# Kernel tuning notes

Measured on AMD Instinct MI355X. Metric: run time of the kernel, lower is better.

## Reference

```python
import jax, jax.numpy as jnp
import numpy as np

N, E, G = 30000, 240000, 128
D_IN, D_H, D_OUT, HEADS = 128, 128, 16, 4
EPS_BN = 1e-5


def setup_inputs() -> dict:
    key = jax.random.key(0)
    ks = jax.random.split(key, 24)
    s = 0.1
    inp = {
        "x": jax.random.normal(ks[0], (N, D_IN), jnp.float32),
        "edge_index": jax.random.randint(ks[1], (2, E), 0, N, jnp.int32),
        "batch": jnp.sort(jax.random.randint(ks[2], (N,), 0, G, jnp.int32)),
        # stacked per-layer params (3 GAT blocks, identical shapes since D_IN==D_H)
        "W": jax.random.normal(ks[3], (3, D_H, HEADS * D_H), jnp.float32) * s,
        "att_src": jax.random.normal(ks[4], (3, HEADS, D_H), jnp.float32) * s,
        "att_dst": jax.random.normal(ks[5], (3, HEADS, D_H), jnp.float32) * s,
        "conv_b": jnp.zeros((3, D_H), jnp.float32),
        "gamma": jnp.ones((3, D_H), jnp.float32),
        "beta": jnp.zeros((3, D_H), jnp.float32),
        "sk_Win": jax.random.normal(ks[6], (3, D_H, D_H), jnp.float32) * s,
        "sk_bin": jnp.zeros((3, D_H), jnp.float32),
        "sk_Wout": jax.random.normal(ks[7], (3, D_H, D_H), jnp.float32) * s,
        "sk_bout": jnp.zeros((3, D_H), jnp.float32),
        "fc1_W": jax.random.normal(ks[8], (D_H, D_H), jnp.float32) * s,
        "fc1_b": jnp.zeros((D_H,), jnp.float32),
        "fc3_W": jax.random.normal(ks[9], (D_H, D_OUT), jnp.float32) * s,
        "fc3_b": jnp.zeros((D_OUT,), jnp.float32),
    }
    return inp


def _gat_conv(x, src, dst, W, a_src, a_dst, b):
    # PyG GATConv, heads=4, concat=False (mean over heads), leaky_relu 0.2
    h = (x @ W).reshape(N, HEADS, D_H)                      # [N,H,C]
    al_s = jnp.einsum('nhc,hc->nh', h, a_src)               # [N,H]
    al_d = jnp.einsum('nhc,hc->nh', h, a_dst)
    e = jax.nn.leaky_relu(al_s[src] + al_d[dst], 0.2)       # [Etot,H]
    m = jax.ops.segment_max(e, dst, num_segments=N)
    m = jnp.where(jnp.isfinite(m), m, 0.0)
    ex = jnp.exp(e - m[dst])
    z = jax.ops.segment_sum(ex, dst, num_segments=N)
    alpha = ex / (z[dst] + 1e-16)                           # [Etot,H]
    msg = h[src] * alpha[:, :, None]                        # [Etot,H,C]
    out = jax.ops.segment_sum(msg, dst, num_segments=N)     # [N,H,C]
    return out.mean(axis=1) + b


def _batch_norm(h, gamma, beta):
    mu = h.mean(axis=0)
    var = h.var(axis=0)
    return gamma * (h - mu) * jax.lax.rsqrt(var + EPS_BN) + beta


def _gated_skip(in_x, out_x, Win, bin_, Wout, bout):
    gate = jax.nn.sigmoid(in_x @ Win + bin_ + out_x @ Wout + bout)
    return gate * out_x + (1.0 - gate) * in_x


def reference(x, edge_index, batch, W, att_src, att_dst, conv_b, gamma, beta,
              sk_Win, sk_bin, sk_Wout, sk_bout, fc1_W, fc1_b, fc3_W, fc3_b):
    # add self loops (PyG GATConv default)
    loops = jnp.arange(N, dtype=edge_index.dtype)
    src = jnp.concatenate([edge_index[0], loops])
    dst = jnp.concatenate([edge_index[1], loops])

    h = x
    for l in range(3):
        idn = h
        h = _gat_conv(h, src, dst, W[l], att_src[l], att_dst[l], conv_b[l])
        h = _batch_norm(h, gamma[l], beta[l])
        h = _gated_skip(idn, h, sk_Win[l], sk_bin[l], sk_Wout[l], sk_bout[l])
        h = jax.nn.relu(h)

    # global mean pool over graphs
    cnt = jax.ops.segment_sum(jnp.ones((N,), h.dtype), batch, num_segments=G)
    hg = jax.ops.segment_sum(h, batch, num_segments=G) / jnp.maximum(cnt, 1.0)[:, None]
    hg = jax.nn.relu(hg @ fc1_W + fc1_b)
    return hg @ fc3_W + fc3_b
```

## Files before the change

### kernel.cpp

```cpp
#include <hip/hip_runtime.h>
#include <hip/hip_bf16.h>

#define N_NODES 30000
#define N_EDGES 240000
#define ETOT    (N_EDGES + N_NODES)
#define NGRAPH  128
#define NBLK    118

typedef __attribute__((ext_vector_type(8))) short bf16x8;
typedef __attribute__((ext_vector_type(4))) short bf16x4;
typedef __attribute__((ext_vector_type(4))) float f32x4;

__device__ __forceinline__ unsigned short f2bf(float f) {
    unsigned u = __float_as_uint(f);
    u += 0x7fff + ((u >> 16) & 1);
    return (unsigned short)(u >> 16);
}
__device__ __forceinline__ float bf2f(unsigned short h) {
    return __uint_as_float(((unsigned)h) << 16);
}

__global__ __launch_bounds__(256) void prep_kernel(const float* __restrict__ W,
                                                   const float* __restrict__ Win,
                                                   const float* __restrict__ Wout,
                                                   const float* __restrict__ x,
                                                   const int* __restrict__ batch,
                                                   short* __restrict__ wt_hi,
                                                   short* __restrict__ wint_hi,
                                                   short* __restrict__ woutt_hi,
                                                   short* __restrict__ xb,
                                                   int* __restrict__ gstart) {
    int i = blockIdx.x * 256 + threadIdx.x;
    if (i < 196608) {
        int l = i >> 16, r = i & 65535;
        int n = r >> 7, k = r & 127;
        wt_hi[i] = (short)f2bf(W[(size_t)l * 65536 + k * 512 + n]);
    } else if (i < 245760) {
        int j = i - 196608;
        int l = j >> 14, r = j & 16383;
        int n = r >> 7, k = r & 127;
        wint_hi[j] = (short)f2bf(Win[(size_t)l * 16384 + k * 128 + n]);
    } else if (i < 294912) {
        int j = i - 245760;
        int l = j >> 14, r = j & 16383;
        int n = r >> 7, k = r & 127;
        woutt_hi[j] = (short)f2bf(Wout[(size_t)l * 16384 + k * 128 + n]);
    } else if (i < 294912 + 480000) {
        int j = i - 294912;
        const float4* p = (const float4*)x + (size_t)j * 2;
        float4 v0 = p[0], v1 = p[1];
        bf16x8 hv;
        hv[0] = (short)f2bf(v0.x); hv[1] = (short)f2bf(v0.y);
        hv[2] = (short)f2bf(v0.z); hv[3] = (short)f2bf(v0.w);
        hv[4] = (short)f2bf(v1.x); hv[5] = (short)f2bf(v1.y);
        hv[6] = (short)f2bf(v1.z); hv[7] = (short)f2bf(v1.w);
        *(bf16x8*)(xb + (size_t)j * 8) = hv;
    } else if (i < 294912 + 480000 + 129) {
        int t = i - 294912 - 480000;
        int lo = 0, hi = N_NODES;
        while (lo < hi) { int mid = (lo + hi) >> 1; if (batch[mid] < t) lo = mid + 1; else hi = mid; }
        gstart[t] = lo;
    }
}

__global__ __launch_bounds__(256) void gemm_conv(const short* __restrict__ Ab,
                                                 const short* __restrict__ Bth,
                                                 const float* __restrict__ att_s,
                                                 const float* __restrict__ att_d,
                                                 unsigned short* __restrict__ hfullb,
                                                 float* __restrict__ als,
                                                 float* __restrict__ ald) {
    __shared__ short As_h[64 * 136];
    __shared__ float red_s[2][64], red_d[2][64];
    const int bm = blockIdx.x * 64;
    const int hd = blockIdx.y;
    const int bn = hd * 128;
    const int t  = threadIdx.x;
#pragma unroll
    for (int i = 0; i < 4; i++) {
        int idx8 = t + i * 256;
        int row = idx8 >> 4, c8 = (idx8 & 15) << 3;
        bf16x8 vh = {};
        if (bm + row < N_NODES)
            vh = *(const bf16x8*)(Ab + (size_t)(bm + row) * 128 + c8);
        *(bf16x8*)(As_h + row * 136 + c8) = vh;
    }
    __syncthreads();

    const int w = t >> 6, lane = t & 63;
    const int wr = w >> 1, wc = w & 1;
    const int lr = lane & 15, lg = lane >> 4;
    f32x4 acc[2][4] = {};
    const size_t bofs0 = (size_t)(bn + wc * 64 + lr) * 128 + lg * 8;
#pragma unroll
    for (int kk = 0; kk < 4; kk++) {
        bf16x8 ah[2], bh[4];
#pragma unroll
        for (int ni = 0; ni < 4; ni++) {
            size_t o = bofs0 + (size_t)ni * 16 * 128 + kk * 32;
            bh[ni] = *(const bf16x8*)(Bth + o);
        }
        int ko = kk * 32 + lg * 8;
#pragma unroll
        for (int mi = 0; mi < 2; mi++) {
            int r = wr * 32 + mi * 16 + lr;
            ah[mi] = *(const bf16x8*)(As_h + r * 136 + ko);
        }
#pragma unroll
        for (int mi = 0; mi < 2; mi++)
#pragma unroll
            for (int ni = 0; ni < 4; ni++)
                acc[mi][ni] = __builtin_amdgcn_mfma_f32_16x16x32_bf16(ah[mi], bh[ni], acc[mi][ni], 0, 0, 0);
    }
    float as_c[4], ad_c[4];
#pragma unroll
    for (int ni = 0; ni < 4; ni++) {
        int cc = wc * 64 + ni * 16 + lr;
        as_c[ni] = att_s[hd * 128 + cc];
        ad_c[ni] = att_d[hd * 128 + cc];
    }
#pragma unroll
    for (int mi = 0; mi < 2; mi++) {
#pragma unroll
        for (int r = 0; r < 4; r++) {
            float ps = 0.f, pd = 0.f;
#pragma unroll
            for (int ni = 0; ni < 4; ni++) {
                ps = fmaf(acc[mi][ni][r], as_c[ni], ps);
                pd = fmaf(acc[mi][ni][r], ad_c[ni], pd);
            }
#pragma unroll
            for (int off = 1; off < 16; off <<= 1) {
                ps += __shfl_xor(ps, off);
                pd += __shfl_xor(pd, off);
            }
            if (lr == 0) {
                int row = wr * 32 + mi * 16 + lg * 4 + r;
                red_s[wc][row] = ps;
                red_d[wc][row] = pd;
            }
        }
    }
    __syncthreads();
#pragma unroll
    for (int mi = 0; mi < 2; mi++)
#pragma unroll
        for (int ni = 0; ni < 4; ni++) {
            int nl = wc * 64 + ni * 16 + lr;
#pragma unroll
            for (int r = 0; r < 4; r++) {
                int row = wr * 32 + mi * 16 + lg * 4 + r;
                As_h[row * 136 + nl] = (short)f2bf(acc[mi][ni][r]);
            }
        }
    if (t < 64) {
        int m = bm + t;
        if (m < N_NODES) als[m * 4 + hd] = red_s[0][t] + red_s[1][t];
    } else if (t < 128) {
        int tt = t - 64;
        int m = bm + tt;
        if (m < N_NODES) ald[m * 4 + hd] = red_d[0][tt] + red_d[1][tt];
    }
    __syncthreads();
#pragma unroll
    for (int i2 = 0; i2 < 4; i2++) {
        int idx8 = t + i2 * 256;
        int row = idx8 >> 4, c8 = (idx8 & 15) << 3;
        int m = bm + row;
        if (m < N_NODES)
            *(bf16x8*)(hfullb + (size_t)m * 512 + bn + c8) = *(const bf16x8*)(As_h + row * 136 + c8);
    }
}

__global__ __launch_bounds__(256) void skip_conv(const short* __restrict__ hinb,
                                                 const float* __restrict__ g,
                                                 const float* __restrict__ bnsum,
                                                 const float* __restrict__ gamma,
                                                 const float* __restrict__ beta,
                                                 const short* __restrict__ w1h,
                                                 const short* __restrict__ w2h,
                                                 const float* __restrict__ bin,
                                                 const float* __restrict__ bout,
                                                 const short* __restrict__ wtn,
                                                 const float* __restrict__ att_s,
                                                 const float* __restrict__ att_d,
                                                 short* __restrict__ houtb,
                                                 unsigned short* __restrict__ hfullb,
                                                 float* __restrict__ als,
                                                 float* __restrict__ ald) {
    __shared__ short A1h[64 * 136], A2h[64 * 136];
    __shared__ float bnp_s[256];
    __shared__ float redS[4][64], redD[4][64];
    const int bm = blockIdx.x * 64;
    const int t  = threadIdx.x;
    if (t < 128) {
        float inv = 1.f / (float)N_NODES;
        float mu  = bnsum[t] * inv;
        float var = bnsum[128 + t] * inv - mu * mu;
        float rs  = rsqrtf(var + 1e-5f);
        float sc  = gamma[t] * rs;
        bnp_s[t]       = sc;
        bnp_s[128 + t] = beta[t] - mu * sc;
    }
    __syncthreads();
#pragma unroll
    for (int i = 0; i < 4; i++) {
        int idx8 = t + i * 256;
        int row = idx8 >> 4, c8 = (idx8 & 15) << 3;
        bf16x8 vh = {};
        if (bm + row < N_NODES)
            vh = *(const bf16x8*)(hinb + (size_t)(bm + row) * 128 + c8);
        *(bf16x8*)(A1h + row * 136 + c8) = vh;
    }
#pragma unroll
    for (int i = 0; i < 8; i++) {
        int idx4 = t + i * 256;
        int row = idx4 >> 5, c4 = (idx4 & 31) << 2;
        float4 v2 = make_float4(0.f, 0.f, 0.f, 0.f);
        if (bm + row < N_NODES) {
            float4 gv = *(const float4*)(g + (size_t)(bm + row) * 128 + c4);
            v2.x = fmaf(bnp_s[c4 + 0], gv.x, bnp_s[128 + c4 + 0]);
            v2.y = fmaf(bnp_s[c4 + 1], gv.y, bnp_s[128 + c4 + 1]);
            v2.z = fmaf(bnp_s[c4 + 2], gv.z, bnp_s[128 + c4 + 2]);
            v2.w = fmaf(bnp_s[c4 + 3], gv.w, bnp_s[128 + c4 + 3]);
        }
        *(bf16x4*)(A2h + row * 136 + c4) = (bf16x4){(short)f2bf(v2.x), (short)f2bf(v2.y),
                                                    (short)f2bf(v2.z), (short)f2bf(v2.w)};
    }
    __syncthreads();

    const int w = t >> 6, lane = t & 63;
    const int wr = w >> 1, wc = w & 1;
    const int lr = lane & 15, lg = lane >> 4;

    {
        f32x4 acc[2][4] = {};
        const size_t bo = (size_t)(wc * 64 + lr) * 128 + lg * 8;
#pragma unroll
        for (int kk = 0; kk < 4; kk++) {
            bf16x8 a1[2], a2[2], b1[4], b2[4];
#pragma unroll
            for (int ni = 0; ni < 4; ni++) {
                size_t o = bo + (size_t)ni * 2048 + kk * 32;
                b1[ni] = *(const bf16x8*)(w1h + o);
                b2[ni] = *(const bf16x8*)(w2h + o);
            }
            int ko = kk * 32 + lg * 8;
#pragma unroll
            for (int mi = 0; mi < 2; mi++) {
                int r = wr * 32 + mi * 16 + lr;
                a1[mi] = *(const bf16x8*)(A1h + r * 136 + ko);
                a2[mi] = *(const bf16x8*)(A2h + r * 136 + ko);
            }
#pragma unroll
            for (int mi = 0; mi < 2; mi++)
#pragma unroll
                for (int ni = 0; ni < 4; ni++) {
                    acc[mi][ni] = __builtin_amdgcn_mfma_f32_16x16x32_bf16(a1[mi], b1[ni], acc[mi][ni], 0, 0, 0);
                    acc[mi][ni] = __builtin_amdgcn_mfma_f32_16x16x32_bf16(a2[mi], b2[ni], acc[mi][ni], 0, 0, 0);
                }
        }
#pragma unroll
        for (int mi = 0; mi < 2; mi++)
#pragma unroll
            for (int ni = 0; ni < 4; ni++) {
                int n = wc * 64 + ni * 16 + lr;
                float bsum = bin[n] + bout[n];
                float sc = bnp_s[n], shb = bnp_s[128 + n];
#pragma unroll
                for (int r = 0; r < 4; r++) {
                    int lrow = wr * 32 + mi * 16 + lg * 4 + r;
                    int m = bm + lrow;
                    float gv = (m < N_NODES) ? g[(size_t)m * 128 + n] : 0.f;
                    float hbnv = fmaf(sc, gv, shb);
                    float hv   = bf2f((unsigned short)A1h[lrow * 136 + n]);
                    float gt   = 1.f / (1.f + __expf(-(acc[mi][ni][r] + bsum)));
                    acc[mi][ni][r] = fmaxf(gt * hbnv + (1.f - gt) * hv, 0.f);
                }
            }
        __syncthreads();
#pragma unroll
        for (int mi = 0; mi < 2; mi++)
#pragma unroll
            for (int ni = 0; ni < 4; ni++) {
                int n = wc * 64 + ni * 16 + lr;
#pragma unroll
                for (int r = 0; r < 4; r++) {
                    int lrow = wr * 32 + mi * 16 + lg * 4 + r;
                    A1h[lrow * 136 + n] = (short)f2bf(acc[mi][ni][r]);
                }
            }
        __syncthreads();
#pragma unroll
        for (int i2 = 0; i2 < 4; i2++) {
            int idx8 = t + i2 * 256;
            int row = idx8 >> 4, c8 = (idx8 & 15) << 3;
            int m = bm + row;
            if (m < N_NODES)
                *(bf16x8*)(houtb + (size_t)m * 128 + c8) = *(const bf16x8*)(A1h + row * 136 + c8);
        }
    }

    f32x4 c2[4][8] = {};
    const int hd = w;
    const size_t bo2 = (size_t)(hd * 128 + lr) * 128 + lg * 8;
#pragma unroll
    for (int kk = 0; kk < 4; kk++) {
        bf16x8 ah2[4], bh2[8];
#pragma unroll
        for (int ni = 0; ni < 8; ni++)
            bh2[ni] = *(const bf16x8*)(wtn + bo2 + (size_t)ni * 2048 + kk * 32);
        int ko = kk * 32 + lg * 8;
#pragma unroll
        for (int mi = 0; mi < 4; mi++)
            ah2[mi] = *(const bf16x8*)(A1h + (mi * 16 + lr) * 136 + ko);
#pragma unroll
        for (int mi = 0; mi < 4; mi++)
#pragma unroll
            for (int ni = 0; ni < 8; ni++)
                c2[mi][ni] = __builtin_amdgcn_mfma_f32_16x16x32_bf16(ah2[mi], bh2[ni], c2[mi][ni], 0, 0, 0);
    }
    {
        float asc[8], adc[8];
#pragma unroll
        for (int ni = 0; ni < 8; ni++) {
            int cc = ni * 16 + lr;
            asc[ni] = att_s[hd * 128 + cc];
            adc[ni] = att_d[hd * 128 + cc];
        }
#pragma unroll
        for (int mi = 0; mi < 4; mi++)
#pragma unroll
            for (int r = 0; r < 4; r++) {
                float ps = 0.f, pd = 0.f;
#pragma unroll
                for (int ni = 0; ni < 8; ni++) {
                    ps = fmaf(c2[mi][ni][r], asc[ni], ps);
                    pd = fmaf(c2[mi][ni][r], adc[ni], pd);
                }
#pragma unroll
                for (int off = 1; off < 16; off <<= 1) {
                    ps += __shfl_xor(ps, off);
                    pd += __shfl_xor(pd, off);
                }
                if (lr == 0) {
                    int row = mi * 16 + lg * 4 + r;
                    redS[hd][row] = ps;
                    redD[hd][row] = pd;
                }
            }
    }
    __syncthreads();
    if (w < 2) {
        short* dst = (w == 0) ? A1h : A2h;
#pragma unroll
        for (int mi = 0; mi < 4; mi++)
#pragma unroll
            for (int ni = 0; ni < 8; ni++)
#pragma unroll
                for (int r = 0; r < 4; r++)
                    dst[(mi * 16 + lg * 4 + r) * 136 + ni * 16 + lr] = (short)f2bf(c2[mi][ni][r]);
    }
    {
        int hd2 = t >> 6, row = t & 63;
        int m = bm + row;
        if (m < N_NODES) {
            als[m * 4 + hd2] = redS[hd2][row];
            ald[m * 4 + hd2] = redD[hd2][row];
        }
    }
    __syncthreads();
#pragma unroll
    for (int it = 0; it < 8; it++) {
        int idx = t + it * 256;
        int row = idx >> 5, c8 = (idx & 31) << 3;
        int m = bm + row;
        if (m < N_NODES) {
            const short* src = (c8 < 128) ? A1h : A2h;
            *(bf16x8*)(hfullb + (size_t)m * 512 + c8) = *(const bf16x8*)(src + row * 136 + (c8 & 127));
        }
    }
    __syncthreads();
    if (w >= 2) {
        short* dst = (w == 2) ? A1h : A2h;
#pragma unroll
        for (int mi = 0; mi < 4; mi++)
#pragma unroll
            for (int ni = 0; ni < 8; ni++)
#pragma unroll
                for (int r = 0; r < 4; r++)
                    dst[(mi * 16 + lg * 4 + r) * 136 + ni * 16 + lr] = (short)f2bf(c2[mi][ni][r]);
    }
    __syncthreads();
#pragma unroll
    for (int it = 0; it < 8; it++) {
        int idx = t + it * 256;
        int row = idx >> 5, c8 = (idx & 31) << 3;
        int m = bm + row;
        if (m < N_NODES) {
            const short* src = (c8 < 128) ? A1h : A2h;
            *(bf16x8*)(hfullb + (size_t)m * 512 + 256 + c8) = *(const bf16x8*)(src + row * 136 + (c8 & 127));
        }
    }
}

__global__ __launch_bounds__(256) void skip_gate(const short* __restrict__ hinb,
                                                 const float* __restrict__ g,
                                                 const float* __restrict__ bnsum,
                                                 const float* __restrict__ gamma,
                                                 const float* __restrict__ beta,
                                                 const short* __restrict__ w1h,
                                                 const short* __restrict__ w2h,
                                                 const float* __restrict__ bin, const float* __restrict__ bout,
                                                 short* __restrict__ houtb) {
    __shared__ short A1h[64 * 136], A2h[64 * 136], A2l[64 * 136];
    __shared__ float bnp_s[256];
    const int bm = blockIdx.x * 64;
    const int bn = blockIdx.y * 64;
    const int t  = threadIdx.x;
    if (t < 128) {
        float inv = 1.f / (float)N_NODES;
        float mu  = bnsum[t] * inv;
        float var = bnsum[128 + t] * inv - mu * mu;
        float rs  = rsqrtf(var + 1e-5f);
        float sc  = gamma[t] * rs;
        bnp_s[t]       = sc;
        bnp_s[128 + t] = beta[t] - mu * sc;
    }
    __syncthreads();
#pragma unroll
    for (int i = 0; i < 4; i++) {
        int idx8 = t + i * 256;
        int row = idx8 >> 4, c8 = (idx8 & 15) << 3;
        bf16x8 vh = {};
        if (bm + row < N_NODES)
            vh = *(const bf16x8*)(hinb + (size_t)(bm + row) * 128 + c8);
        *(bf16x8*)(A1h + row * 136 + c8) = vh;
    }
#pragma unroll
    for (int i = 0; i < 8; i++) {
        int idx4 = t + i * 256;
        int row = idx4 >> 5, c4 = (idx4 & 31) << 2;
        float4 v2 = make_float4(0.f, 0.f, 0.f, 0.f);
        if (bm + row < N_NODES) {
            float4 gv = *(const float4*)(g + (size_t)(bm + row) * 128 + c4);
            v2.x = fmaf(bnp_s[c4 + 0], gv.x, bnp_s[128 + c4 + 0]);
            v2.y = fmaf(bnp_s[c4 + 1], gv.y, bnp_s[128 + c4 + 1]);
            v2.z = fmaf(bnp_s[c4 + 2], gv.z, bnp_s[128 + c4 + 2]);
            v2.w = fmaf(bnp_s[c4 + 3], gv.w, bnp_s[128 + c4 + 3]);
        }
        unsigned short b0 = f2bf(v2.x), b1 = f2bf(v2.y), b2 = f2bf(v2.z), b3 = f2bf(v2.w);
        *(bf16x4*)(A2h + row * 136 + c4) = (bf16x4){(short)b0, (short)b1, (short)b2, (short)b3};
        *(bf16x4*)(A2l + row * 136 + c4) = (bf16x4){(short)f2bf(v2.x - bf2f(b0)), (short)f2bf(v2.y - bf2f(b1)),
                                                    (short)f2bf(v2.z - bf2f(b2)), (short)f2bf(v2.w - bf2f(b3))};
    }
    __syncthreads();

    const int w = t >> 6, lane = t & 63;
    const int wr = w >> 1, wc = w & 1;
    const int lr = lane & 15, lg = lane >> 4;
    f32x4 acc[2][2] = {};
    const size_t bofs0 = (size_t)(bn + wc * 32 + lr) * 128 + lg * 8;
#pragma unroll
    for (int kk = 0; kk < 4; kk++) {
        bf16x8 a1f[2], a2f[2], b1h[2], b2h[2];
#pragma unroll
        for (int ni = 0; ni < 2; ni++) {
            size_t o = bofs0 + (size_t)ni * 16 * 128 + kk * 32;
            b1h[ni] = *(const bf16x8*)(w1h + o);
            b2h[ni] = *(const bf16x8*)(w2h + o);
        }
        int ko = kk * 32 + lg * 8;
#pragma unroll
        for (int mi = 0; mi < 2; mi++) {
            int r = wr * 32 + mi * 16 + lr;
            a1f[mi] = *(const bf16x8*)(A1h + r * 136 + ko);
            a2f[mi] = *(const bf16x8*)(A2h + r * 136 + ko);
        }
#pragma unroll
        for (int mi = 0; mi < 2; mi++)
#pragma unroll
            for (int ni = 0; ni < 2; ni++) {
                acc[mi][ni] = __builtin_amdgcn_mfma_f32_16x16x32_bf16(a1f[mi], b1h[ni], acc[mi][ni], 0, 0, 0);
                acc[mi][ni] = __builtin_amdgcn_mfma_f32_16x16x32_bf16(a2f[mi], b2h[ni], acc[mi][ni], 0, 0, 0);
            }
    }
#pragma unroll
    for (int mi = 0; mi < 2; mi++) {
#pragma unroll
        for (int ni = 0; ni < 2; ni++) {
            int n = bn + wc * 32 + ni * 16 + lr;
            float bsum = bin[n] + bout[n];
#pragma unroll
            for (int r = 0; r < 4; r++) {
                int lrow = wr * 32 + mi * 16 + lg * 4 + r;
                float hbnv = bf2f((unsigned short)A2h[lrow * 136 + n]) + bf2f((unsigned short)A2l[lrow * 136 + n]);
                float hv   = bf2f((unsigned short)A1h[lrow * 136 + n]);
                float gt   = 1.f / (1.f + __expf(-(acc[mi][ni][r] + bsum)));
                acc[mi][ni][r] = fmaxf(gt * hbnv + (1.f - gt) * hv, 0.f);
            }
        }
    }
    __syncthreads();
#pragma unroll
    for (int mi = 0; mi < 2; mi++)
#pragma unroll
        for (int ni = 0; ni < 2; ni++) {
            int n = bn + wc * 32 + ni * 16 + lr;
#pragma unroll
            for (int r = 0; r < 4; r++) {
                int lrow = wr * 32 + mi * 16 + lg * 4 + r;
                A1h[lrow * 136 + n] = (short)f2bf(acc[mi][ni][r]);
            }
        }
    __syncthreads();
#pragma unroll
    for (int i2 = 0; i2 < 2; i2++) {
        int idx8 = t + i2 * 256;
        int row = idx8 >> 3, c8 = (idx8 & 7) << 3;
        int m = bm + row;
        if (m < N_NODES)
            *(bf16x8*)(houtb + (size_t)m * 128 + bn + c8) = *(const bf16x8*)(A1h + row * 136 + bn + c8);
    }
}

__global__ __launch_bounds__(256) void deg_kernel(const int* __restrict__ ei1,
                                                  int* __restrict__ deg) {
    int e = blockIdx.x * 256 + threadIdx.x;
    if (e >= ETOT) return;
    int d = (e < N_EDGES) ? ei1[e] : (e - N_EDGES);
    atomicAdd(&deg[d], 1);
}

__global__ __launch_bounds__(256) void scan1(const int* __restrict__ deg,
                                             int* __restrict__ tmp,
                                             int* __restrict__ blksum) {
    int i = blockIdx.x * 256 + threadIdx.x;
    int v = (i < N_NODES) ? deg[i] : 0;
    __shared__ int sh[256];
    sh[threadIdx.x] = v;
    __syncthreads();
    int acc = v;
    for (int off = 1; off < 256; off <<= 1) {
        int u = (threadIdx.x >= off) ? sh[threadIdx.x - off] : 0;
        __syncthreads();
        acc += u;
        sh[threadIdx.x] = acc;
        __syncthreads();
    }
    if (i < N_NODES) tmp[i] = acc - v;
    if (threadIdx.x == 255) blksum[blockIdx.x] = acc;
}

__global__ void scan2(const int* __restrict__ blksum, int* __restrict__ blkoff) {
    int t = threadIdx.x;
    int v = (t < NBLK) ? blksum[t] : 0;
    __shared__ int sh[128];
    sh[t] = v;
    __syncthreads();
    int acc = v;
    for (int off = 1; off < 128; off <<= 1) {
        int u = (t >= off) ? sh[t - off] : 0;
        __syncthreads();
        acc += u;
        sh[t] = acc;
        __syncthreads();
    }
    if (t < NBLK) blkoff[t] = acc - v;
}

__global__ __launch_bounds__(256) void scan3(const int* __restrict__ tmp,
                                             const int* __restrict__ blkoff,
                                             int* __restrict__ rowptr,
                                             int* __restrict__ wofs) {
    int i = blockIdx.x * 256 + threadIdx.x;
    if (i == 0) rowptr[N_NODES] = ETOT;
    if (i < N_NODES) {
        int r = tmp[i] + blkoff[blockIdx.x];
        rowptr[i] = r;
        wofs[i]   = r;
    }
}

__global__ __launch_bounds__(256) void scatter_kernel(const int* __restrict__ ei0,
                                                      const int* __restrict__ ei1,
                                                      int* __restrict__ wofs,
                                                      int* __restrict__ csr_src) {
    int e = blockIdx.x * 256 + threadIdx.x;
    if (e >= ETOT) return;
    int s = (e < N_EDGES) ? ei0[e] : (e - N_EDGES);
    int d = (e < N_EDGES) ? ei1[e] : (e - N_EDGES);
    int pos = atomicAdd(&wofs[d], 1);
    csr_src[pos] = s;
}

__global__ __launch_bounds__(256) void gat_gather(const int* __restrict__ rowptr,
                                                  const int* __restrict__ csr_src,
                                                  const float* __restrict__ al_s,
                                                  const float* __restrict__ al_d,
                                                  const unsigned short* __restrict__ hfullb,
                                                  const float* __restrict__ conv_b,
                                                  float* __restrict__ g,
                                                  float* __restrict__ bnsum,
                                                  float* __restrict__ bnsum2) {
    const int lane = threadIdx.x & 63;
    const int wib  = threadIdx.x >> 6;
    const int gwid = blockIdx.x * 4 + wib;
    const int nw   = gridDim.x * 4;
    const int h    = lane >> 4;
    const int sub  = lane & 15;
    float s1[8] = {}, s2[8] = {};

    for (int n = gwid; n < N_NODES; n += nw) {
        const int e0 = rowptr[n], e1 = rowptr[n + 1];
        const float ald_h = al_d[n * 4 + h];

        float acc[8] = {};
        float zs = 0.f;
        int i = e0;
        for (; i + 3 < e1; i += 4) {
            int sA = csr_src[i], sB = csr_src[i + 1], sC = csr_src[i + 2], sD = csr_src[i + 3];
            bf16x8 ha = *(const bf16x8*)(hfullb + (size_t)sA * 512 + lane * 8);
            bf16x8 hb = *(const bf16x8*)(hfullb + (size_t)sB * 512 + lane * 8);
            bf16x8 hc = *(const bf16x8*)(hfullb + (size_t)sC * 512 + lane * 8);
            bf16x8 hd = *(const bf16x8*)(hfullb + (size_t)sD * 512 + lane * 8);
            float vA = al_s[sA * 4 + h] + ald_h; vA = (vA > 0.f) ? vA : 0.2f * vA;
            float vB = al_s[sB * 4 + h] + ald_h; vB = (vB > 0.f) ? vB : 0.2f * vB;
            float vC = al_s[sC * 4 + h] + ald_h; vC = (vC > 0.f) ? vC : 0.2f * vC;
            float vD = al_s[sD * 4 + h] + ald_h; vD = (vD > 0.f) ? vD : 0.2f * vD;
            float exA = __expf(vA), exB = __expf(vB), exC = __expf(vC), exD = __expf(vD);
            zs += (exA + exB) + (exC + exD);
#pragma unroll
            for (int j = 0; j < 8; j++) {
                float a = fmaf(exA, bf2f((unsigned short)ha[j]), acc[j]);
                a = fmaf(exB, bf2f((unsigned short)hb[j]), a);
                a = fmaf(exC, bf2f((unsigned short)hc[j]), a);
                acc[j] = fmaf(exD, bf2f((unsigned short)hd[j]), a);
            }
        }
        for (; i < e1; i++) {
            int sA = csr_src[i];
            bf16x8 ha = *(const bf16x8*)(hfullb + (size_t)sA * 512 + lane * 8);
            float vA = al_s[sA * 4 + h] + ald_h; vA = (vA > 0.f) ? vA : 0.2f * vA;
            float exA = __expf(vA);
            zs += exA;
#pragma unroll
            for (int j = 0; j < 8; j++)
                acc[j] = fmaf(exA, bf2f((unsigned short)ha[j]), acc[j]);
        }

        float inv = 0.25f / (zs + 1e-16f);
#pragma unroll
        for (int j = 0; j < 8; j++) {
            float a = acc[j] * inv;
            a += __shfl_xor(a, 16);
            a += __shfl_xor(a, 32);
            acc[j] = a;
        }
        if (lane < 16) {
            float o[8];
#pragma unroll
            for (int j = 0; j < 8; j++) {
                float tv = acc[j] + conv_b[sub * 8 + j];
                o[j] = tv;
                s1[j] += tv;
                s2[j] = fmaf(tv, tv, s2[j]);
            }
            float* gp = g + (size_t)n * 128 + sub * 8;
            *(float4*)gp       = make_float4(o[0], o[1], o[2], o[3]);
            *(float4*)(gp + 4) = make_float4(o[4], o[5], o[6], o[7]);
        }
    }

    __shared__ float redA[4][128], redB[4][128];
    if (lane < 16) {
#pragma unroll
        for (int j = 0; j < 8; j++) {
            redA[wib][sub * 8 + j] = s1[j];
            redB[wib][sub * 8 + j] = s2[j];
        }
    }
    __syncthreads();
    int t = threadIdx.x;
    if (t < 128) {
        atomicAdd(&bnsum[t], redA[0][t] + redA[1][t] + redA[2][t] + redA[3][t]);
    } else {
        int c = t - 128;
        atomicAdd(&bnsum2[c], redB[0][c] + redB[1][c] + redB[2][c] + redB[3][c]);
    }
}

__global__ __launch_bounds__(256) void pool_head(const short* __restrict__ hb,
                                                 const int* __restrict__ gstart,
                                                 const float* __restrict__ fc1W,
                                                 const float* __restrict__ fc1b,
                                                 const float* __restrict__ fc3W,
                                                 const float* __restrict__ fc3b,
                                                 float* __restrict__ out) {
    int gid = blockIdx.x, t = threadIdx.x;
    int lo = gstart[gid], hi = gstart[gid + 1];
    int c = t & 127, half = t >> 7;
    float s = 0.f;
    for (int n = lo + half; n < hi; n += 2)
        s += bf2f((unsigned short)hb[(size_t)n * 128 + c]);
    __shared__ float sh[256];
    __shared__ float hg[128], a1[128];
    sh[t] = s;
    __syncthreads();
    if (half == 0) {
        float cc = fmaxf((float)(hi - lo), 1.f);
        hg[c] = (sh[c] + sh[c + 128]) / cc;
    }
    __syncthreads();
    if (t < 128) {
        float v = fc1b[t];
        for (int c2 = 0; c2 < 128; c2++) v = fmaf(hg[c2], fc1W[c2 * 128 + t], v);
        a1[t] = fmaxf(v, 0.f);
    }
    __syncthreads();
    if (t < 16) {
        float o = fc3b[t];
        for (int j = 0; j < 128; j++) o = fmaf(a1[j], fc3W[j * 16 + t], o);
        out[gid * 16 + t] = o;
    }
}

extern "C" void kernel_launch(void* const* d_in, const int* in_sizes, int n_in,
                              void* d_out, int out_size, void* d_ws, size_t ws_size,
                              hipStream_t stream) {
    const float* x       = (const float*)d_in[0];
    const int*   ei      = (const int*)d_in[1];
    const int*   batch   = (const int*)d_in[2];
    const float* W       = (const float*)d_in[3];
    const float* att_src = (const float*)d_in[4];
    const float* att_dst = (const float*)d_in[5];
    const float* conv_b  = (const float*)d_in[6];
    const float* gamma   = (const float*)d_in[7];
    const float* beta    = (const float*)d_in[8];
    const float* sk_Win  = (const float*)d_in[9];
    const float* sk_bin  = (const float*)d_in[10];
    const float* sk_Wout = (const float*)d_in[11];
    const float* sk_bout = (const float*)d_in[12];
    const float* fc1_W   = (const float*)d_in[13];
    const float* fc1_b   = (const float*)d_in[14];
    const float* fc3_W   = (const float*)d_in[15];
    const float* fc3_b   = (const float*)d_in[16];
    float* out = (float*)d_out;
    const int* ei0 = ei;
    const int* ei1 = ei + N_EDGES;

    float* ws = (float*)d_ws;
    size_t o = 0;
    unsigned short* hfullb = (unsigned short*)(ws + o); o += (size_t)N_NODES * 256;
    float* gbuf   = ws + o; o += (size_t)N_NODES * 128;
    short* hbA    = (short*)(ws + o); o += (size_t)N_NODES * 64;
    short* hbB    = (short*)(ws + o); o += (size_t)N_NODES * 64;
    float* als    = ws + o; o += N_NODES * 4;
    float* ald    = ws + o; o += N_NODES * 4;
    float* bnsum  = ws + o; o += 768;
    short* wt_hi   = (short*)(ws + o); o += 98304;
    short* wint_hi = (short*)(ws + o); o += 24576;
    short* woutt_hi = (short*)(ws + o); o += 24576;
    int* gstart   = (int*)(ws + o); o += 132;
    int* deg      = (int*)(ws + o); o += N_NODES;
    int* rowptr   = (int*)(ws + o); o += N_NODES + 4;
    int* wofs     = (int*)(ws + o); o += N_NODES;
    int* scantmp  = (int*)(ws + o); o += N_NODES;
    int* blksum   = (int*)(ws + o); o += NBLK + 2;
    int* blkoff   = (int*)(ws + o); o += NBLK + 2;
    int* csr_src  = (int*)(ws + o); o += ETOT;

    prep_kernel<<<3028, 256, 0, stream>>>(W, sk_Win, sk_Wout, x, batch,
                                          wt_hi, wint_hi, woutt_hi, hbA, gstart);

    hipMemsetAsync(deg, 0, N_NODES * 4, stream);
    hipMemsetAsync(bnsum, 0, 768 * 4, stream);
    deg_kernel<<<(ETOT + 255) / 256, 256, 0, stream>>>(ei1, deg);
    scan1<<<NBLK, 256, 0, stream>>>(deg, scantmp, blksum);
    scan2<<<1, 128, 0, stream>>>(blksum, blkoff);
    scan3<<<NBLK, 256, 0, stream>>>(scantmp, blkoff, rowptr, wofs);
    scatter_kernel<<<(ETOT + 255) / 256, 256, 0, stream>>>(ei0, ei1, wofs, csr_src);

    gemm_conv<<<dim3(469, 4), 256, 0, stream>>>(hbA, wt_hi, att_src, att_dst, hfullb, als, ald);
    gat_gather<<<1024, 256, 0, stream>>>(rowptr, csr_src, als, ald, hfullb,
                                         conv_b, gbuf, bnsum, bnsum + 128);
    skip_conv<<<469, 256, 0, stream>>>(hbA, gbuf, bnsum, gamma, beta,
                                       wint_hi, woutt_hi, sk_bin, sk_bout,
                                       wt_hi + 65536, att_src + 512, att_dst + 512,
                                       hbB, hfullb, als, ald);
    gat_gather<<<1024, 256, 0, stream>>>(rowptr, csr_src, als, ald, hfullb,
                                         conv_b + 128, gbuf, bnsum + 256, bnsum + 384);
    skip_conv<<<469, 256, 0, stream>>>(hbB, gbuf, bnsum + 256, gamma + 128, beta + 128,
                                       wint_hi + 16384, woutt_hi + 16384, sk_bin + 128, sk_bout + 128,
                                       wt_hi + 131072, att_src + 1024, att_dst + 1024,
                                       hbA, hfullb, als, ald);
    gat_gather<<<1024, 256, 0, stream>>>(rowptr, csr_src, als, ald, hfullb,
                                         conv_b + 256, gbuf, bnsum + 512, bnsum + 640);
    skip_gate<<<dim3(469, 2), 256, 0, stream>>>(hbA, gbuf, bnsum + 512, gamma + 256, beta + 256,
                                                wint_hi + 32768, woutt_hi + 32768,
                                                sk_bin + 256, sk_bout + 256, hbB);

    pool_head<<<NGRAPH, 256, 0, stream>>>(hbB, gstart, fc1_W, fc1_b, fc3_W, fc3_b, out);
}
```

Baseline: 413.3 us.

## Edge-balance gather waves, fold memsets into prep, widen pool head block

```diff
diff --git a/kernel.cpp b/kernel.cpp
--- a/kernel.cpp
+++ b/kernel.cpp
@@ -6,6 +6,7 @@
 #define ETOT    (N_EDGES + N_NODES)
 #define NGRAPH  128
 #define NBLK    118
+#define NWAVES  4096
 
 typedef __attribute__((ext_vector_type(8))) short bf16x8;
 typedef __attribute__((ext_vector_type(4))) short bf16x4;
@@ -29,7 +30,9 @@
                                                    short* __restrict__ wint_hi,
                                                    short* __restrict__ woutt_hi,
                                                    short* __restrict__ xb,
-                                                   int* __restrict__ gstart) {
+                                                   int* __restrict__ gstart,
+                                                   int* __restrict__ deg,
+                                                   float* __restrict__ bnsum) {
     int i = blockIdx.x * 256 + threadIdx.x;
     if (i < 196608) {
         int l = i >> 16, r = i & 65535;
@@ -45,7 +48,7 @@
         int l = j >> 14, r = j & 16383;
         int n = r >> 7, k = r & 127;
         woutt_hi[j] = (short)f2bf(Wout[(size_t)l * 16384 + k * 128 + n]);
-    } else if (i < 294912 + 480000) {
+    } else if (i < 774912) {
         int j = i - 294912;
         const float4* p = (const float4*)x + (size_t)j * 2;
         float4 v0 = p[0], v1 = p[1];
@@ -55,11 +58,15 @@
         hv[4] = (short)f2bf(v1.x); hv[5] = (short)f2bf(v1.y);
         hv[6] = (short)f2bf(v1.z); hv[7] = (short)f2bf(v1.w);
         *(bf16x8*)(xb + (size_t)j * 8) = hv;
-    } else if (i < 294912 + 480000 + 129) {
-        int t = i - 294912 - 480000;
+    } else if (i < 775041) {
+        int t = i - 774912;
         int lo = 0, hi = N_NODES;
         while (lo < hi) { int mid = (lo + hi) >> 1; if (batch[mid] < t) lo = mid + 1; else hi = mid; }
         gstart[t] = lo;
+    } else if (i < 805041) {
+        deg[i - 775041] = 0;
+    } else if (i < 805809) {
+        bnsum[i - 805041] = 0.f;
     }
 }
 
@@ -582,6 +589,17 @@
     }
 }
 
+__global__ __launch_bounds__(256) void wpart_kernel(const int* __restrict__ rowptr,
+                                                    int* __restrict__ wstart) {
+    int wid = blockIdx.x * 256 + threadIdx.x;
+    if (wid > NWAVES) return;
+    if (wid == NWAVES) { wstart[NWAVES] = N_NODES; return; }
+    int target = (int)(((long)wid * ETOT) / NWAVES);
+    int lo = 0, hi = N_NODES;
+    while (lo < hi) { int mid = (lo + hi) >> 1; if (rowptr[mid] < target) lo = mid + 1; else hi = mid; }
+    wstart[wid] = lo;
+}
+
 __global__ __launch_bounds__(256) void scatter_kernel(const int* __restrict__ ei0,
                                                       const int* __restrict__ ei1,
                                                       int* __restrict__ wofs,
@@ -595,6 +613,7 @@
 }
 
 __global__ __launch_bounds__(256) void gat_gather(const int* __restrict__ rowptr,
+                                                  const int* __restrict__ wstart,
                                                   const int* __restrict__ csr_src,
                                                   const float* __restrict__ al_s,
                                                   const float* __restrict__ al_d,
@@ -606,12 +625,12 @@
     const int lane = threadIdx.x & 63;
     const int wib  = threadIdx.x >> 6;
     const int gwid = blockIdx.x * 4 + wib;
-    const int nw   = gridDim.x * 4;
     const int h    = lane >> 4;
     const int sub  = lane & 15;
     float s1[8] = {}, s2[8] = {};
 
-    for (int n = gwid; n < N_NODES; n += nw) {
+    const int n0 = wstart[gwid], n1 = wstart[gwid + 1];
+    for (int n = n0; n < n1; n++) {
         const int e0 = rowptr[n], e1 = rowptr[n + 1];
         const float ald_h = al_d[n * 4 + h];
 
@@ -690,31 +709,46 @@
     }
 }
 
-__global__ __launch_bounds__(256) void pool_head(const short* __restrict__ hb,
-                                                 const int* __restrict__ gstart,
-                                                 const float* __restrict__ fc1W,
-                                                 const float* __restrict__ fc1b,
-                                                 const float* __restrict__ fc3W,
-                                                 const float* __restrict__ fc3b,
-                                                 float* __restrict__ out) {
+__global__ __launch_bounds__(1024) void pool_head(const short* __restrict__ hb,
+                                                  const int* __restrict__ gstart,
+                                                  const float* __restrict__ fc1W,
+                                                  const float* __restrict__ fc1b,
+                                                  const float* __restrict__ fc3W,
+                                                  const float* __restrict__ fc3b,
+                                                  float* __restrict__ out) {
     int gid = blockIdx.x, t = threadIdx.x;
     int lo = gstart[gid], hi = gstart[gid + 1];
-    int c = t & 127, half = t >> 7;
+    int c = t & 127, q = t >> 7;
     float s = 0.f;
-    for (int n = lo + half; n < hi; n += 2)
+    for (int n = lo + q; n < hi; n += 8)
         s += bf2f((unsigned short)hb[(size_t)n * 128 + c]);
-    __shared__ float sh[256];
+    __shared__ float sh[1024];
     __shared__ float hg[128], a1[128];
     sh[t] = s;
     __syncthreads();
-    if (half == 0) {
+    if (t < 128) {
         float cc = fmaxf((float)(hi - lo), 1.f);
-        hg[c] = (sh[c] + sh[c + 128]) / cc;
+        float tot = 0.f;
+#pragma unroll
+        for (int q2 = 0; q2 < 8; q2++) tot += sh[q2 * 128 + t];
+        hg[t] = tot / cc;
+    }
+    __syncthreads();
+    {
+        int oc = t & 127, ch = t >> 7;
+        float v = 0.f;
+#pragma unroll
+        for (int k = 0; k < 16; k++) {
+            int c2 = ch * 16 + k;
+            v = fmaf(hg[c2], fc1W[c2 * 128 + oc], v);
+        }
+        sh[t] = v;
     }
     __syncthreads();
     if (t < 128) {
         float v = fc1b[t];
-        for (int c2 = 0; c2 < 128; c2++) v = fmaf(hg[c2], fc1W[c2 * 128 + t], v);
+#pragma unroll
+        for (int q2 = 0; q2 < 8; q2++) v += sh[q2 * 128 + t];
         a1[t] = fmaxf(v, 0.f);
     }
     __syncthreads();
@@ -768,37 +802,37 @@
     int* scantmp  = (int*)(ws + o); o += N_NODES;
     int* blksum   = (int*)(ws + o); o += NBLK + 2;
     int* blkoff   = (int*)(ws + o); o += NBLK + 2;
+    int* wstart   = (int*)(ws + o); o += NWAVES + 2;
     int* csr_src  = (int*)(ws + o); o += ETOT;
 
-    prep_kernel<<<3028, 256, 0, stream>>>(W, sk_Win, sk_Wout, x, batch,
-                                          wt_hi, wint_hi, woutt_hi, hbA, gstart);
-
-    hipMemsetAsync(deg, 0, N_NODES * 4, stream);
-    hipMemsetAsync(bnsum, 0, 768 * 4, stream);
+    prep_kernel<<<3148, 256, 0, stream>>>(W, sk_Win, sk_Wout, x, batch,
+                                          wt_hi, wint_hi, woutt_hi, hbA, gstart, deg, bnsum);
+
     deg_kernel<<<(ETOT + 255) / 256, 256, 0, stream>>>(ei1, deg);
     scan1<<<NBLK, 256, 0, stream>>>(deg, scantmp, blksum);
     scan2<<<1, 128, 0, stream>>>(blksum, blkoff);
     scan3<<<NBLK, 256, 0, stream>>>(scantmp, blkoff, rowptr, wofs);
+    wpart_kernel<<<17, 256, 0, stream>>>(rowptr, wstart);
     scatter_kernel<<<(ETOT + 255) / 256, 256, 0, stream>>>(ei0, ei1, wofs, csr_src);
 
     gemm_conv<<<dim3(469, 4), 256, 0, stream>>>(hbA, wt_hi, att_src, att_dst, hfullb, als, ald);
-    gat_gather<<<1024, 256, 0, stream>>>(rowptr, csr_src, als, ald, hfullb,
+    gat_gather<<<1024, 256, 0, stream>>>(rowptr, wstart, csr_src, als, ald, hfullb,
                                          conv_b, gbuf, bnsum, bnsum + 128);
     skip_conv<<<469, 256, 0, stream>>>(hbA, gbuf, bnsum, gamma, beta,
                                        wint_hi, woutt_hi, sk_bin, sk_bout,
                                        wt_hi + 65536, att_src + 512, att_dst + 512,
                                        hbB, hfullb, als, ald);
-    gat_gather<<<1024, 256, 0, stream>>>(rowptr, csr_src, als, ald, hfullb,
+    gat_gather<<<1024, 256, 0, stream>>>(rowptr, wstart, csr_src, als, ald, hfullb,
                                          conv_b + 128, gbuf, bnsum + 256, bnsum + 384);
     skip_conv<<<469, 256, 0, stream>>>(hbB, gbuf, bnsum + 256, gamma + 128, beta + 128,
                                        wint_hi + 16384, woutt_hi + 16384, sk_bin + 128, sk_bout + 128,
                                        wt_hi + 131072, att_src + 1024, att_dst + 1024,
                                        hbA, hfullb, als, ald);
-    gat_gather<<<1024, 256, 0, stream>>>(rowptr, csr_src, als, ald, hfullb,
+    gat_gather<<<1024, 256, 0, stream>>>(rowptr, wstart, csr_src, als, ald, hfullb,
                                          conv_b + 256, gbuf, bnsum + 512, bnsum + 640);
     skip_gate<<<dim3(469, 2), 256, 0, stream>>>(hbA, gbuf, bnsum + 512, gamma + 256, beta + 256,
                                                 wint_hi + 32768, woutt_hi + 32768,
                                                 sk_bin + 256, sk_bout + 256, hbB);
 
-    pool_head<<<NGRAPH, 256, 0, stream>>>(hbB, gstart, fc1_W, fc1_b, fc3_W, fc3_b, out);
-}
+    pool_head<<<NGRAPH, 1024, 0, stream>>>(hbB, gstart, fc1_W, fc1_b, fc3_W, fc3_b, out);
+}
```

Measured after the change: 390.0 us. 1.06x faster.
